# Kernel tuning notes

Measured on AMD Instinct MI355X. Metric: run time of the kernel, lower is better.

The kernel has to match this reference:

```python
import jax, jax.numpy as jnp
import numpy as np

T, B, N = 12, 2, 1024
M = B * N            # nodes per timestep (batch-flattened)
D_IN, D_H, D_T, D_O = 64, 128, 16, 32


def _linear_params(k, fin, fout):
    kw, kb = jax.random.split(k)
    s = 1.0 / np.sqrt(fin)
    w = jax.random.uniform(kw, (fin, fout), jnp.float32, -s, s)
    b = jax.random.uniform(kb, (fout,), jnp.float32, -s, s)
    return w, b


def setup_inputs() -> dict:
    key = jax.random.key(0)
    ks = jax.random.split(key, 12)
    x = jax.random.normal(ks[0], (T, M, D_IN), jnp.float32)
    A = (jax.random.uniform(ks[1], (T, M, M)) < 0.01).astype(jnp.float32)
    A = A * (1.0 - jnp.eye(M, dtype=jnp.float32))  # no self-loops in raw adjacency
    ego_mask = jax.random.randint(ks[2], (B, T, N), 0, 2).astype(bool)
    gcn1_w, gcn1_b = _linear_params(ks[3], D_IN, D_H)
    gcn2_w, gcn2_b = _linear_params(ks[4], D_H, D_H)
    time_w, time_b = _linear_params(ks[5], 1, D_T)
    q_w, q_b = _linear_params(ks[6], D_H + D_T, D_H)
    k_w, k_b = _linear_params(ks[7], D_H + D_T, D_H)
    v_w, v_b = _linear_params(ks[8], D_H + D_T, D_H)
    o_w, o_b = _linear_params(ks[9], D_H, D_H)
    fc_w, fc_b = _linear_params(ks[10], D_H, D_O)
    return dict(x=x, A=A, ego_mask=ego_mask,
                gcn1_w=gcn1_w, gcn1_b=gcn1_b, gcn2_w=gcn2_w, gcn2_b=gcn2_b,
                time_w=time_w, time_b=time_b,
                q_w=q_w, q_b=q_b, k_w=k_w, k_b=k_b, v_w=v_w, v_b=v_b,
                o_w=o_w, o_b=o_b, fc_w=fc_w, fc_b=fc_b)


def _forward(x, A, ego_mask, gcn1_w, gcn1_b, gcn2_w, gcn2_b, time_w, time_b,
             q_w, q_b, k_w, k_b, v_w, v_b, o_w, o_b, fc_w, fc_b):
    # [B,T,N] -> [T, B*N], as in mask.permute(1,0,2).reshape(T,-1)
    mask = ego_mask.transpose(1, 0, 2).reshape(T, M)
    tvals = jnp.arange(T, dtype=jnp.float32)

    def step(_, inp):
        xt, At, mt, tv = inp  # [M,D_IN], [M,M], [M] bool, scalar
        m = mt.astype(xt.dtype)
        # restrict adjacency to masked subgraph; GCNConv adds self-loops
        A_hat = At * (m[:, None] * m[None, :]) + jnp.diag(m)
        deg = A_hat.sum(axis=0)  # in-degree per target (PyG gcn_norm on col)
        nrm = jnp.where(deg > 0, 1.0 / jnp.sqrt(jnp.maximum(deg, 1e-12)), 0.0)

        def gcn(h, w, b):
            # out[i] = nrm[i] * sum_j A_hat[j,i] * nrm[j] * (hW)[j] + b
            return (A_hat.T @ ((h @ w) * nrm[:, None])) * nrm[:, None] + b

        h = jax.nn.relu(gcn(xt, gcn1_w, gcn1_b))
        h = jax.nn.relu(gcn(h, gcn2_w, gcn2_b))
        # t_vec = sin(Linear(1,D_T)(t)) -- identical for all nodes
        t_vec = jnp.sin(tv * time_w[0] + time_b)  # [D_T]
        xtc = jnp.concatenate([h, jnp.broadcast_to(t_vec, (M, D_T))], axis=-1)
        Q = xtc @ q_w + q_b
        K = xtc @ k_w + k_b
        V = xtc @ v_w + v_b
        scores = (Q @ K.T) * (1.0 / np.sqrt(D_H))  # [M,M]
        scores = jnp.where(mt[None, :], scores, -1e9)  # keys restricted to mask
        agg = jax.nn.softmax(scores, axis=-1) @ V
        out = ((agg @ o_w + o_b) @ fc_w + fc_b) * m[:, None]  # scatter-back == mask
        return None, out

    _, outs = jax.lax.scan(step, None, (x, A, mask, tvals))  # [T,M,D_O]
    return outs.reshape(T, B, N, D_O).transpose(1, 2, 0, 3)  # [B,N,T,D_O]


def reference(x, A, ego_mask, gcn1_w, gcn1_b, gcn2_w, gcn2_b, time_w, time_b,
              q_w, q_b, k_w, k_b, v_w, v_b, o_w, o_b, fc_w, fc_b):
    return _forward(x, A, ego_mask, gcn1_w, gcn1_b, gcn2_w, gcn2_b, time_w,
                    time_b, q_w, q_b, k_w, k_b, v_w, v_b, o_w, o_b, fc_w, fc_b)
```

## Files before the change

kernel.cpp:

```cpp
#include <hip/hip_runtime.h>
#include <stdint.h>

#define TT   12
#define BB   2
#define NN   1024
#define MM   2048
#define TM   24576
#define DIN  64
#define DH   128
#define DOUT 32
#define CAP  64
#define OUTSZ 786432
#define PWB  292

typedef __attribute__((ext_vector_type(8))) short short8;
typedef __attribute__((ext_vector_type(4))) short short4v;
typedef __attribute__((ext_vector_type(4))) float f32x4;

#define MFMA(a,b,c) __builtin_amdgcn_mfma_f32_16x16x32_bf16((a),(b),(c),0,0,0)

__device__ __forceinline__ float bf2f(unsigned short u){
  union { uint32_t i; float f; } x; x.i = ((uint32_t)u) << 16; return x.f;
}
__device__ __forceinline__ unsigned short f2bf(float f){
  union { float f; uint32_t i; } x; x.f = f;
  uint32_t u = x.i + 0x7FFFu + ((x.i >> 16) & 1u);
  return (unsigned short)(u >> 16);
}
__device__ __forceinline__ float LD(const void* p, size_t i, int mode){
  return mode ? ((const float*)p)[i] : bf2f(((const unsigned short*)p)[i]);
}
__device__ __forceinline__ short8 ldx8(const void* x, size_t off, int md){
  if(md){
    const float4* xf = (const float4*)((const float*)x + off);
    float4 a = xf[0], b = xf[1];
    short8 o;
    o[0]=(short)f2bf(a.x); o[1]=(short)f2bf(a.y); o[2]=(short)f2bf(a.z); o[3]=(short)f2bf(a.w);
    o[4]=(short)f2bf(b.x); o[5]=(short)f2bf(b.y); o[6]=(short)f2bf(b.z); o[7]=(short)f2bf(b.w);
    return o;
  }
  return *(const short8*)((const unsigned short*)x + off);
}

__global__ void k_fill(float* __restrict__ out, int n, float val){
  int i = blockIdx.x*blockDim.x + threadIdx.x;
  if(i < n) out[i] = val;
}

__global__ __launch_bounds__(256) void k_maskdet(
    const void* __restrict__ egom, const unsigned short* __restrict__ xs,
    int* __restrict__ dtf,
    int* __restrict__ cnt, int* __restrict__ nact,
    int* __restrict__ aidx, int* __restrict__ inv,
    float* __restrict__ out)
{
  const int bid = blockIdx.x, tid = threadIdx.x;
  out[(size_t)bid*256 + tid] = 0.f;
  if(bid > TT) return;
  if(bid == TT){
    __shared__ int cnt_s;
    if(tid == 0) cnt_s = 0;
    __syncthreads();
    int c = 0;
    for(int i = tid; i < 6144; i += 256){
      unsigned short hh = xs[i*2];
      unsigned e = (hh >> 7) & 0xFF;
      if(hh==0 || (e >= 0x60 && e <= 0x9F)) c++;
    }
    if(c) atomicAdd(&cnt_s, c);
    __syncthreads();
    if(tid == 0) *dtf = (cnt_s > 4000) ? 0 : 1;
    return;
  }
  const int t = bid, lane = tid & 63, wv = tid >> 6;

  __shared__ int pres_s, ge2_s, wcnt_s[4];
  if(tid == 0){ pres_s = 0; ge2_s = 0; }
  __syncthreads();
  {
    int pres = 0, ge2 = 0;
    const unsigned char* egp = (const unsigned char*)egom;
    for(int i = tid; i < 24576; i += 256){
      unsigned v = egp[i];
      if(v){ pres |= 1 << (i & 7); if(v >= 2u) ge2 = 1; }
    }
    if(pres) atomicOr(&pres_s, pres);
    if(ge2)  atomicOr(&ge2_s, 1);
  }
  __syncthreads();
  int mode;
  {
    int pr = pres_s, g2 = ge2_s;
    if(!g2){
      if((pr & ~0x01) == 0)      mode = 4;
      else if((pr & ~0x11) == 0) mode = 0;
      else                       mode = 1;
    } else {
      if((pr & ~0xC0) == 0)      mode = 5;
      else if((pr & ~0xCC) == 0) mode = 3;
      else                       mode = 2;
    }
  }

  int base = 0;
  for(int r = 0; r < 8; r++){
    int node = r*256 + tid;
    int b = node / NN, n = node % NN;
    int src = (b*TT + t)*NN + n;
    int v;
    if(mode==0)      v = ((const int*)egom)[src] != 0;
    else if(mode==1) v = ((const unsigned char*)egom)[src] != 0;
    else if(mode==2) v = ((const unsigned short*)egom)[src] != 0;
    else if(mode==3) v = ((const float*)egom)[src] != 0.f;
    else if(mode==4) v = ((const long long*)egom)[src] != 0;
    else             v = ((const double*)egom)[src] != 0.0;
    cnt[(size_t)t*MM + node] = 0;
    unsigned long long bal = __ballot(v != 0);
    if(lane == 0) wcnt_s[wv] = __popcll(bal);
    __syncthreads();
    int mybase = base;
    for(int w2 = 0; w2 < wv; w2++) mybase += wcnt_s[w2];
    int ic = -1;
    if(v){
      ic = mybase + __popcll(bal & ((1ULL << lane) - 1ULL));
      aidx[(size_t)t*MM + ic] = node;
    }
    inv[(size_t)t*MM + node] = ic;
    base += wcnt_s[0] + wcnt_s[1] + wcnt_s[2] + wcnt_s[3];
    __syncthreads();
  }
  if(tid == 0) nact[t] = base;
}


__device__ __forceinline__ void dev_prepw2_item(int id, int md,
  const void* w2,
  const void* qw, const void* kw, const void* vw,
  const void* qb0, const void* kb0, const void* vb0,
  const void* ow, const void* ob, const void* fw, const void* fb,
  const void* tw, const void* tb, const void* b1, const void* b2,
  unsigned short* W2t,
  unsigned short* Wqt, unsigned short* Wkt,
  unsigned short* Wvt, unsigned short* Wct,
  float* qbf, float* kbf, float* vbf,
  float* bcf, float* b1f, float* b2f)
{
  if(id < 16384){ int n=id&127,k2=id>>7; W2t[n*128+k2]=f2bf(LD(w2,(size_t)k2*128+n,md)); return; }
  id -= 16384;
  if(id < 16384){ int n=id&127,k2=id>>7; Wqt[n*128+k2]=f2bf(LD(qw,(size_t)k2*128+n,md)); return; }
  id -= 16384;
  if(id < 16384){ int n=id&127,k2=id>>7; Wkt[n*128+k2]=f2bf(LD(kw,(size_t)k2*128+n,md)); return; }
  id -= 16384;
  if(id < 16384){ int n=id&127,k2=id>>7; Wvt[n*128+k2]=f2bf(LD(vw,(size_t)k2*128+n,md)); return; }
  id -= 16384;
  if(id < 4096){
    int oc=id&31, c=id>>5; float s=0.f;
    for(int r=0;r<128;r++) s += LD(ow,(size_t)c*128+r,md)*LD(fw,(size_t)r*32+oc,md);
    Wct[oc*128+c]=f2bf(s); return;
  }
  id -= 4096;
  if(id < 32){
    float s = LD(fb,id,md);
    for(int r=0;r<128;r++) s += LD(ob,r,md)*LD(fw,(size_t)r*32+id,md);
    bcf[id]=s; return;
  }
  id -= 32;
  if(id < 4608){
    int which = id/1536, rem=id%1536, t=rem/128, n=rem%128;
    const void* W  = which==0?qw:(which==1?kw:vw);
    const void* Bs = which==0?qb0:(which==1?kb0:vb0);
    float s = LD(Bs,n,md);
    for(int d=0;d<16;d++){
      float tv = sinf((float)t*LD(tw,d,md) + LD(tb,d,md));
      s += tv * LD(W,(size_t)(128+d)*128+n,md);
    }
    float* dst = which==0?qbf:(which==1?kbf:vbf);
    dst[t*128+n]=s; return;
  }
  id -= 4608;
  if(id < 256){
    if(id<128) b1f[id] = LD(b1,id,md);
    else       b2f[id-128] = LD(b2,id-128,md);
    return;
  }
}

__device__ __forceinline__ void dev_edges_item(int id, int md,
    const void* A, const int* inv, int* cnt, int* edges){
  int lane = id & 63; int row = id >> 6;
  int t = row / MM;
  int jc = inv[row];
  if(jc < 0) return;
  const int* invt = inv + (size_t)t*MM;
  int* cb = cnt + (size_t)t*MM;
  int* eb = edges + (size_t)t*MM*CAP;
  if(md){
    const float4* p4 = (const float4*)((const float*)A + (size_t)row*MM);
    #pragma unroll
    for(int u=0;u<8;u++){
      float4 v = p4[u*64 + lane];
      float wd[4]={v.x,v.y,v.z,v.w};
      #pragma unroll
      for(int q=0;q<4;q++){
        if(wd[q]!=0.f){
          int ibc = invt[(u*64 + lane)*4 + q];
          if(ibc >= 0){ int s=atomicAdd(&cb[ibc],1); if(s<CAP) eb[(size_t)ibc*CAP+s]=jc; }
        }
      }
    }
  } else {
    const uint4* p4 = (const uint4*)((const unsigned short*)A + (size_t)row*MM);
    #pragma unroll
    for(int u=0;u<4;u++){
      uint4 v = p4[u*64 + lane];
      unsigned wd[4]={v.x,v.y,v.z,v.w};
      #pragma unroll
      for(int q=0;q<4;q++){
        int ib = (u*64 + lane)*8 + q*2;
        if(wd[q] & 0xFFFFu){
          int ibc = invt[ib];
          if(ibc >= 0){ int s=atomicAdd(&cb[ibc],1); if(s<CAP) eb[(size_t)ibc*CAP+s]=jc; }
        }
        if(wd[q] >> 16){
          int ibc = invt[ib+1];
          if(ibc >= 0){ int s=atomicAdd(&cb[ibc],1); if(s<CAP) eb[(size_t)ibc*CAP+s]=jc; }
        }
      }
    }
  }
}

__device__ __forceinline__ void dev_gemm_x_direct(int tileIdx, int md, int tid,
    const void* x, const int* nact, const int* aidx,
    const void* w1, float* g)
{
  const int tile = tileIdx*64;
  const int t = tile / MM, il = tile % MM;
  const int na = nact[t];
  if(il >= ((na+63)&~63)) return;
  const int wv=tid>>6, lane=tid&63, l15=lane&15, quad=lane>>4;
  const int r0 = tile + (wv>>1)*32;
  const int c0 = (wv&1)*64;
  short8 bf[2][4];
  #pragma unroll
  for(int kk=0;kk<2;kk++)
    #pragma unroll
    for(int nt=0;nt<4;nt++){
      const int col = c0+nt*16+l15;
      short8 o;
      #pragma unroll
      for(int j=0;j<8;j++)
        o[j] = (short)f2bf(LD(w1, (size_t)(kk*32 + quad*8 + j)*DH + col, md));
      bf[kk][nt] = o;
    }
  const int il0 = (r0 % MM) + l15, il1 = (r0 % MM) + 16 + l15;
  const int n0 = aidx[(size_t)t*MM + (il0 < na ? il0 : 0)];
  const int n1 = aidx[(size_t)t*MM + (il1 < na ? il1 : 0)];
  const size_t xb0 = ((size_t)t*MM + n0)*DIN;
  const size_t xb1 = ((size_t)t*MM + n1)*DIN;
  f32x4 z = {0.f,0.f,0.f,0.f};
  f32x4 acc[2][4];
  #pragma unroll
  for(int i=0;i<2;i++){ acc[i][0]=z; acc[i][1]=z; acc[i][2]=z; acc[i][3]=z; }
  #pragma unroll
  for(int kk=0;kk<2;kk++){
    short8 a0 = ldx8(x, xb0 + kk*32 + quad*8, md);
    short8 a1 = ldx8(x, xb1 + kk*32 + quad*8, md);
    #pragma unroll
    for(int nt=0;nt<4;nt++){
      acc[0][nt]=MFMA(a0,bf[kk][nt],acc[0][nt]);
      acc[1][nt]=MFMA(a1,bf[kk][nt],acc[1][nt]);
    }
  }
  #pragma unroll
  for(int mt=0;mt<2;mt++)
    #pragma unroll
    for(int nt=0;nt<4;nt++){
      int col = c0+nt*16+l15;
      #pragma unroll
      for(int r=0;r<4;r++){
        int row = r0 + mt*16 + quad*4 + r;
        g[(size_t)row*DH + col] = acc[mt][nt][r];
      }
    }
}

__global__ __launch_bounds__(256) void k_pex(
  const void* __restrict__ x, const void* __restrict__ A,
  const void* __restrict__ w1, const void* __restrict__ w2,
  const void* __restrict__ qw, const void* __restrict__ kw, const void* __restrict__ vw,
  const void* __restrict__ qb0, const void* __restrict__ kb0, const void* __restrict__ vb0,
  const void* __restrict__ ow, const void* __restrict__ ob,
  const void* __restrict__ fw, const void* __restrict__ fb,
  const void* __restrict__ tw, const void* __restrict__ tb,
  const void* __restrict__ b1, const void* __restrict__ b2,
  const int* __restrict__ dtf,
  const int* __restrict__ inv, int* __restrict__ cnt, int* __restrict__ edges,
  const int* __restrict__ nact, const int* __restrict__ aidx, float* __restrict__ g,
  unsigned short* __restrict__ W2t,
  unsigned short* __restrict__ Wqt, unsigned short* __restrict__ Wkt,
  unsigned short* __restrict__ Wvt, unsigned short* __restrict__ Wct,
  float* __restrict__ qbf, float* __restrict__ kbf, float* __restrict__ vbf,
  float* __restrict__ bcf, float* __restrict__ b1f, float* __restrict__ b2f)
{
  const int tid = threadIdx.x;
  const int md = *dtf;
  const int b = blockIdx.x;
  if(b < PWB){
    dev_prepw2_item(b*256 + tid, md, w2, qw,kw,vw, qb0,kb0,vb0, ow,ob,fw,fb, tw,tb, b1,b2,
                    W2t, Wqt, Wkt, Wvt, Wct, qbf, kbf, vbf, bcf, b1f, b2f);
  } else if(b < PWB + TM*64/256){
    dev_edges_item((b - PWB)*256 + tid, md, A, inv, cnt, edges);
  } else {
    dev_gemm_x_direct(b - PWB - TM*64/256, md, tid, x, nact, aidx, w1, g);
  }
}

__global__ __launch_bounds__(256) void k_gemm_h(const unsigned short* __restrict__ X,
    const unsigned short* __restrict__ Wt, float* __restrict__ g,
    const int* __restrict__ nact)
{
  const int tile = blockIdx.x*64;
  const int t = tile / MM, il = tile % MM;
  const int na = nact[t];
  if(il >= ((na+63)&~63)) return;
  const int tid=threadIdx.x, wv=tid>>6, lane=tid&63, l15=lane&15, quad=lane>>4;
  const int r0 = tile + (wv>>1)*32;
  const int c0 = (wv&1)*64;
  short8 bf[4][4];
  #pragma unroll
  for(int kk=0;kk<4;kk++)
    #pragma unroll
    for(int nt=0;nt<4;nt++)
      bf[kk][nt] = *(const short8*)(Wt + (size_t)(c0+nt*16+l15)*DH + kk*32 + quad*8);
  f32x4 z = {0.f,0.f,0.f,0.f};
  f32x4 acc[2][4];
  #pragma unroll
  for(int i=0;i<2;i++){ acc[i][0]=z; acc[i][1]=z; acc[i][2]=z; acc[i][3]=z; }
  #pragma unroll
  for(int kk=0;kk<4;kk++){
    short8 a0 = *(const short8*)(X + (size_t)(r0+l15)*DH    + kk*32 + quad*8);
    short8 a1 = *(const short8*)(X + (size_t)(r0+16+l15)*DH + kk*32 + quad*8);
    #pragma unroll
    for(int nt=0;nt<4;nt++){
      acc[0][nt]=MFMA(a0,bf[kk][nt],acc[0][nt]);
      acc[1][nt]=MFMA(a1,bf[kk][nt],acc[1][nt]);
    }
  }
  #pragma unroll
  for(int mt=0;mt<2;mt++)
    #pragma unroll
    for(int nt=0;nt<4;nt++){
      int col = c0+nt*16+l15;
      #pragma unroll
      for(int r=0;r<4;r++){
        int row = r0 + mt*16 + quad*4 + r;
        g[(size_t)row*DH + col] = acc[mt][nt][r];
      }
    }
}

__global__ __launch_bounds__(256) void k_gather(const float* __restrict__ g,
    const int* __restrict__ edges, const int* __restrict__ cnt,
    const int* __restrict__ nact, const float* __restrict__ bias,
    unsigned short* __restrict__ h)
{
  int wv = threadIdx.x>>6, lane = threadIdx.x&63;
  int gi = blockIdx.x*4 + wv;
  int t = gi / MM, ic = gi % MM;
  int na = nact[t];
  if(ic >= ((na+63)&~63)) return;
  unsigned int* hp = (unsigned int*)(h + (size_t)gi*DH) + lane;
  if(ic >= na){ *hp = 0; return; }
  float a0=0.f, a1=0.f;
  int cn = cnt[gi]; if(cn>CAP) cn=CAP;
  const int* eb = edges + (size_t)gi*CAP;
  #pragma unroll 2
  for(int e=0;e<cn;e++){
    int jc = eb[e];
    float nj = rsqrtf((float)cnt[(size_t)t*MM+jc] + 1.f);
    float2 gr2 = *(const float2*)(g + ((size_t)t*MM + jc)*DH + 2*lane);
    a0 += nj*gr2.x; a1 += nj*gr2.y;
  }
  float ni = rsqrtf((float)cn + 1.f);
  float2 gs2 = *(const float2*)(g + (size_t)gi*DH + 2*lane);
  float h0 = ni*(a0 + ni*gs2.x) + bias[2*lane];
  float h1 = ni*(a1 + ni*gs2.y) + bias[2*lane+1];
  h0 = h0>0.f?h0:0.f; h1 = h1>0.f?h1:0.f;
  *hp = (unsigned int)f2bf(h0) | ((unsigned int)f2bf(h1) << 16);
}

__global__ __launch_bounds__(256) void k_gemm_qkv(const unsigned short* __restrict__ X,
    const unsigned short* __restrict__ Wq, const unsigned short* __restrict__ Wk,
    const unsigned short* __restrict__ Wv,
    const float* __restrict__ qb, const float* __restrict__ kb, const float* __restrict__ vb,
    unsigned short* __restrict__ Qo, unsigned short* __restrict__ Ko,
    unsigned short* __restrict__ Vtc, const int* __restrict__ nact)
{
  const int tile = blockIdx.x*64;
  const int t = tile / MM, il = tile % MM;
  const int na = nact[t];
  if(il >= ((na+63)&~63)) return;
  const int which = blockIdx.z;
  const unsigned short* Wt = which==0?Wq:(which==1?Wk:Wv);
  const float* bias = which==0?qb:(which==1?kb:vb);
  const int tid=threadIdx.x, wv=tid>>6, lane=tid&63, l15=lane&15, quad=lane>>4;
  const int r0 = tile + (wv>>1)*32;
  const int c0 = (wv&1)*64;
  short8 bf[4][4];
  #pragma unroll
  for(int kk=0;kk<4;kk++)
    #pragma unroll
    for(int nt=0;nt<4;nt++)
      bf[kk][nt] = *(const short8*)(Wt + (size_t)(c0+nt*16+l15)*DH + kk*32 + quad*8);
  f32x4 z = {0.f,0.f,0.f,0.f};
  f32x4 acc[2][4];
  #pragma unroll
  for(int i=0;i<2;i++){ acc[i][0]=z; acc[i][1]=z; acc[i][2]=z; acc[i][3]=z; }
  #pragma unroll
  for(int kk=0;kk<4;kk++){
    short8 a0 = *(const short8*)(X + (size_t)(r0+l15)*DH    + kk*32 + quad*8);
    short8 a1 = *(const short8*)(X + (size_t)(r0+16+l15)*DH + kk*32 + quad*8);
    #pragma unroll
    for(int nt=0;nt<4;nt++){
      acc[0][nt]=MFMA(a0,bf[kk][nt],acc[0][nt]);
      acc[1][nt]=MFMA(a1,bf[kk][nt],acc[1][nt]);
    }
  }
  if(which < 2){
    unsigned short* o = which==0 ? Qo : Ko;
    #pragma unroll
    for(int mt=0;mt<2;mt++)
      #pragma unroll
      for(int nt=0;nt<4;nt++){
        int col = c0+nt*16+l15;
        float bb = bias[t*DH+col];
        #pragma unroll
        for(int r=0;r<4;r++){
          int row = r0 + mt*16 + quad*4 + r;
          o[(size_t)row*DH + col] = f2bf(acc[mt][nt][r] + bb);
        }
      }
  } else {
    #pragma unroll
    for(int mt=0;mt<2;mt++)
      #pragma unroll
      for(int nt=0;nt<4;nt++){
        int col = c0+nt*16+l15;
        float bb = bias[t*DH+col];
        int node0 = il + (wv>>1)*32 + mt*16 + quad*4;
        short4v pk;
        #pragma unroll
        for(int r=0;r<4;r++) pk[r] = (short)f2bf(acc[mt][nt][r] + bb);
        *(short4v*)(Vtc + ((size_t)t*DH + col)*MM + node0) = pk;
      }
  }
}

__global__ __launch_bounds__(256) void k_attn(
  const unsigned short* __restrict__ Q, const unsigned short* __restrict__ Kc,
  const unsigned short* __restrict__ Vtc, const int* __restrict__ nact,
  const int* __restrict__ aidx, const unsigned short* __restrict__ Wct,
  const float* __restrict__ bc, float* __restrict__ out)
{
  __shared__ unsigned short Kl[64][136];
  __shared__ unsigned short Vl[128][72];
  __shared__ short Pl[4][16][72];
  __shared__ short Al[4][16][136];
  const int tid=threadIdx.x, wv=tid>>6, lane=tid&63, l15=lane&15, quad=lane>>4;
  const int t = blockIdx.y;
  const int na = nact[t];
  const int qblk = blockIdx.x*64;
  if(qblk >= na) return;
  const int qbase = qblk + wv*16;
  const float scale = 0.088388347648318447f;
  const int nkt = (na + 63) >> 6;

  short8 bq[4];
  #pragma unroll
  for(int kk=0;kk<4;kk++)
    bq[kk] = *(const short8*)(Q + ((size_t)t*MM + qbase + l15)*DH + kk*32 + quad*8);

  f32x4 zz = {0.f,0.f,0.f,0.f};
  f32x4 accPV[8];
  #pragma unroll
  for(int i=0;i<8;i++) accPV[i]=zz;
  float l_run = 0.f;

  const int srow = tid >> 2, sseg = tid & 3;
  const int vch  = tid >> 1, vhalf = tid & 1;

  short8 kreg[4], vreg[4];
  {
    const unsigned short* gk = Kc + ((size_t)t*MM + srow)*DH + sseg*32;
    const unsigned short* gv = Vtc + ((size_t)t*DH + vch)*MM + vhalf*32;
    #pragma unroll
    for(int j=0;j<4;j++){ kreg[j] = *(const short8*)(gk + j*8);
                          vreg[j] = *(const short8*)(gv + j*8); }
  }

  for(int kt=0; kt<nkt; kt++){
    const int key0 = kt*64;
    __syncthreads();
    {
      short8* kd = (short8*)&Kl[srow][sseg*32];
      short8* vd = (short8*)&Vl[vch][vhalf*32];
      #pragma unroll
      for(int j=0;j<4;j++){ kd[j] = kreg[j]; vd[j] = vreg[j]; }
    }
    __syncthreads();
    if(kt+1 < nkt){
      const int key1 = key0 + 64;
      const unsigned short* gk = Kc + ((size_t)t*MM + key1 + srow)*DH + sseg*32;
      const unsigned short* gv = Vtc + ((size_t)t*DH + vch)*MM + key1 + vhalf*32;
      #pragma unroll
      for(int j=0;j<4;j++){ kreg[j] = *(const short8*)(gk + j*8);
                            vreg[j] = *(const short8*)(gv + j*8); }
    }
    #pragma unroll
    for(int mt=0;mt<4;mt++){
      f32x4 s = zz;
      #pragma unroll
      for(int kk=0;kk<4;kk++){
        short8 ak = *(const short8*)&Kl[mt*16+l15][kk*32 + quad*8];
        s = MFMA(ak, bq[kk], s);
      }
      short4v pk;
      #pragma unroll
      for(int r=0;r<4;r++){
        float sv = fminf(fmaxf(s[r]*scale, -15.f), 15.f);
        float valid = (key0 + mt*16 + quad*4 + r < na) ? 1.f : 0.f;
        float p = __expf(sv) * valid;
        pk[r] = (short)f2bf(p);
        l_run += bf2f((unsigned short)pk[r]);
      }
      *(short4v*)&Pl[wv][l15][mt*16 + quad*4] = pk;
    }
    #pragma unroll
    for(int kk=0;kk<2;kk++){
      short8 ap = *(const short8*)&Pl[wv][l15][kk*32 + quad*8];
      #pragma unroll
      for(int nt=0;nt<8;nt++){
        short8 bv = *(const short8*)&Vl[nt*16+l15][kk*32 + quad*8];
        accPV[nt] = MFMA(ap, bv, accPV[nt]);
      }
    }
  }
  l_run += __shfl_xor(l_run, 16, 64);
  l_run += __shfl_xor(l_run, 32, 64);

  #pragma unroll
  for(int nt=0;nt<8;nt++)
    #pragma unroll
    for(int r=0;r<4;r++){
      float av = fminf(fmaxf(accPV[nt][r], -1e30f), 1e30f);
      Al[wv][quad*4+r][nt*16+l15] = (short)f2bf(av);
    }

  const int qc = qbase + l15;
  const bool qok = (qc < na);
  const float linv = (l_run > 0.f) ? 1.f/l_run : 0.f;
  const int node = aidx[(size_t)t*MM + (qok ? qc : 0)];
  #pragma unroll
  for(int mt2=0;mt2<2;mt2++){
    f32x4 d = zz;
    #pragma unroll
    for(int kk=0;kk<4;kk++){
      short8 aw = *(const short8*)(Wct + (size_t)(mt2*16+l15)*DH + kk*32 + quad*8);
      short8 bl = *(const short8*)&Al[wv][l15][kk*32 + quad*8];
      d = MFMA(aw, bl, d);
    }
    f32x4 bcv = *(const f32x4*)(bc + mt2*16 + quad*4);
    f32x4 o4;
    #pragma unroll
    for(int r=0;r<4;r++) o4[r] = d[r]*linv + bcv[r];
    if(qok)
      *(f32x4*)(out + (size_t)node*(TT*DOUT) + (size_t)t*DOUT + mt2*16 + quad*4) = o4;
  }
}


extern "C" void kernel_launch(void* const* d_in, const int* in_sizes, int n_in,
                              void* d_out, int out_size, void* d_ws, size_t ws_size,
                              hipStream_t stream)
{
  float* outp = (float*)d_out;
  static const int EXP[19] = {1572864,50331648,24576,8192,128,16384,128,16,16,
                              18432,128,18432,128,18432,128,16384,128,4096,32};
  bool ok = (n_in >= 19) && (out_size == OUTSZ);
  if(ok) for(int i=0;i<19;i++) if(in_sizes[i] != EXP[i]) { ok = false; break; }
  if(!ok){
    k_fill<<<(out_size+255)/256,256,0,stream>>>(outp, out_size, 1000.f);
    return;
  }
  const void* x   = d_in[0];
  const void* A   = d_in[1];
  const void* eg  = d_in[2];
  const void* w1  = d_in[3];
  const void* b1  = d_in[4];
  const void* w2  = d_in[5];
  const void* b2  = d_in[6];
  const void* tw  = d_in[7];
  const void* tb  = d_in[8];
  const void* qw  = d_in[9];
  const void* qb0 = d_in[10];
  const void* kw  = d_in[11];
  const void* kb0 = d_in[12];
  const void* vw  = d_in[13];
  const void* vb0 = d_in[14];
  const void* ow  = d_in[15];
  const void* ob  = d_in[16];
  const void* fw  = d_in[17];
  const void* fb  = d_in[18];

  char* w = (char*)d_ws;
  size_t off = 0;
  auto alloc = [&](size_t sz)->char*{
    char* p = w + off; off = (off + sz + 255) & ~(size_t)255; return p; };
  int*   dtf   = (int*)  alloc(4);
  int*   nactb = (int*)  alloc(TT*4);
  int*   cnt   = (int*)  alloc((size_t)TM*4);
  int*   aidx  = (int*)  alloc((size_t)TM*4);
  int*   inv   = (int*)  alloc((size_t)TM*4);
  int*   edges = (int*)  alloc((size_t)TM*CAP*4);
  float* g     = (float*)alloc((size_t)TM*DH*4);
  unsigned short* h   = (unsigned short*)alloc((size_t)TM*DH*2);
  unsigned short* Vtc = (unsigned short*)alloc((size_t)TT*DH*MM*2);
  unsigned short* W2t = (unsigned short*)alloc(DH*DH*2);
  unsigned short* Wqt = (unsigned short*)alloc(DH*DH*2);
  unsigned short* Wkt = (unsigned short*)alloc(DH*DH*2);
  unsigned short* Wvt = (unsigned short*)alloc(DH*DH*2);
  unsigned short* Wct = (unsigned short*)alloc(DOUT*DH*2);
  float* qbf = (float*)alloc(TT*DH*4);
  float* kbf = (float*)alloc(TT*DH*4);
  float* vbf = (float*)alloc(TT*DH*4);
  float* bcf = (float*)alloc(DOUT*4);
  float* b1f = (float*)alloc(DH*4);
  float* b2f = (float*)alloc(DH*4);
  if(off > ws_size){
    k_fill<<<(out_size+255)/256,256,0,stream>>>(outp, out_size, 500.f);
    return;
  }

  unsigned short* Qb = (unsigned short*)g;
  unsigned short* Kb = (unsigned short*)((char*)g + (size_t)TM*DH*2);

  k_maskdet<<<OUTSZ/256,256,0,stream>>>(eg, (const unsigned short*)x, dtf,
                                        cnt, nactb, aidx, inv, outp);
  k_pex<<<PWB + TM*64/256 + TM/64,256,0,stream>>>(
      x, A, w1, w2, qw, kw, vw, qb0, kb0, vb0, ow, ob, fw, fb, tw, tb, b1, b2,
      dtf, inv, cnt, edges, nactb, aidx, g,
      W2t, Wqt, Wkt, Wvt, Wct, qbf, kbf, vbf, bcf, b1f, b2f);
  k_gather<<<TM/4,256,0,stream>>>(g, edges, cnt, nactb, b1f, h);
  k_gemm_h<<<TM/64,256,0,stream>>>(h, W2t, g, nactb);
  k_gather<<<TM/4,256,0,stream>>>(g, edges, cnt, nactb, b2f, h);
  k_gemm_qkv<<<dim3(TM/64,1,3),256,0,stream>>>(h, Wqt,Wkt,Wvt, qbf,kbf,vbf, Qb,Kb,Vtc, nactb);
  k_attn<<<dim3(MM/64,TT),256,0,stream>>>(Qb, Kb, Vtc, nactb, aidx, Wct, bcf, outp);
}
```

Measured before the change: 473.3 us.

## Fuse GCN gather into following GEMMs via LDS tiles and merge QKV passes

```diff
diff --git a/kernel.cpp b/kernel.cpp
--- a/kernel.cpp
+++ b/kernel.cpp
@@ -51,12 +51,9 @@
     const void* __restrict__ egom, const unsigned short* __restrict__ xs,
     int* __restrict__ dtf,
     int* __restrict__ cnt, int* __restrict__ nact,
-    int* __restrict__ aidx, int* __restrict__ inv,
-    float* __restrict__ out)
+    int* __restrict__ aidx, int* __restrict__ inv)
 {
   const int bid = blockIdx.x, tid = threadIdx.x;
-  out[(size_t)bid*256 + tid] = 0.f;
-  if(bid > TT) return;
   if(bid == TT){
     __shared__ int cnt_s;
     if(tid == 0) cnt_s = 0;
@@ -316,16 +313,56 @@
   }
 }
 
-__global__ __launch_bounds__(256) void k_gemm_h(const unsigned short* __restrict__ X,
-    const unsigned short* __restrict__ Wt, float* __restrict__ g,
-    const int* __restrict__ nact)
-{
+__device__ __forceinline__ void dev_gather_tile(int tile, int t, int il, int na,
+    int tid, const float* __restrict__ gsrc, const int* __restrict__ edges,
+    const int* __restrict__ cnt, const float* __restrict__ bias,
+    unsigned short (*Hl)[136])
+{
+  const int wv = tid>>6, lane = tid&63;
+  for(int r = 0; r < 16; r++){
+    const int lrow = wv*16 + r;
+    const int ic = il + lrow;
+    const int gi = t*MM + ic;
+    float h0 = 0.f, h1 = 0.f;
+    if(ic < na){
+      float a0=0.f, a1=0.f;
+      int cn = cnt[gi]; if(cn>CAP) cn=CAP;
+      const int* eb = edges + (size_t)gi*CAP;
+      #pragma unroll 4
+      for(int e=0;e<cn;e++){
+        int jc = eb[e];
+        float nj = rsqrtf((float)cnt[(size_t)t*MM+jc] + 1.f);
+        float2 gr2 = *(const float2*)(gsrc + ((size_t)t*MM + jc)*DH + 2*lane);
+        a0 += nj*gr2.x; a1 += nj*gr2.y;
+      }
+      float ni = rsqrtf((float)cn + 1.f);
+      float2 gs2 = *(const float2*)(gsrc + (size_t)gi*DH + 2*lane);
+      h0 = ni*(a0 + ni*gs2.x) + bias[2*lane];
+      h1 = ni*(a1 + ni*gs2.y) + bias[2*lane+1];
+      h0 = h0>0.f?h0:0.f; h1 = h1>0.f?h1:0.f;
+    }
+    *(unsigned int*)&Hl[lrow][2*lane] =
+        (unsigned int)f2bf(h0) | ((unsigned int)f2bf(h1) << 16);
+  }
+}
+
+__global__ __launch_bounds__(256) void k_gg1(
+    const float* __restrict__ g, const int* __restrict__ edges,
+    const int* __restrict__ cnt, const int* __restrict__ nact,
+    const float* __restrict__ bias, const unsigned short* __restrict__ Wt,
+    float* __restrict__ g2)
+{
+  __shared__ unsigned short Hl[64][136];
+  const int tid = threadIdx.x, wv = tid>>6, lane = tid&63, l15 = lane&15, quad = lane>>4;
   const int tile = blockIdx.x*64;
   const int t = tile / MM, il = tile % MM;
   const int na = nact[t];
   if(il >= ((na+63)&~63)) return;
-  const int tid=threadIdx.x, wv=tid>>6, lane=tid&63, l15=lane&15, quad=lane>>4;
-  const int r0 = tile + (wv>>1)*32;
+
+  dev_gather_tile(tile, t, il, na, tid, g, edges, cnt, bias, Hl);
+  __syncthreads();
+
+  const int r0l = (wv>>1)*32;
   const int c0 = (wv&1)*64;
   short8 bf[4][4];
   #pragma unroll
@@ -339,8 +376,8 @@
   for(int i=0;i<2;i++){ acc[i][0]=z; acc[i][1]=z; acc[i][2]=z; acc[i][3]=z; }
   #pragma unroll
   for(int kk=0;kk<4;kk++){
-    short8 a0 = *(const short8*)(X + (size_t)(r0+l15)*DH    + kk*32 + quad*8);
-    short8 a1 = *(const short8*)(X + (size_t)(r0+16+l15)*DH + kk*32 + quad*8);
+    short8 a0 = *(const short8*)&Hl[r0l+l15   ][kk*32 + quad*8];
+    short8 a1 = *(const short8*)&Hl[r0l+16+l15][kk*32 + quad*8];
     #pragma unroll
     for(int nt=0;nt<4;nt++){
       acc[0][nt]=MFMA(a0,bf[kk][nt],acc[0][nt]);
@@ -354,113 +391,93 @@
       int col = c0+nt*16+l15;
       #pragma unroll
       for(int r=0;r<4;r++){
-        int row = r0 + mt*16 + quad*4 + r;
-        g[(size_t)row*DH + col] = acc[mt][nt][r];
-      }
-    }
-}
-
-__global__ __launch_bounds__(256) void k_gather(const float* __restrict__ g,
-    const int* __restrict__ edges, const int* __restrict__ cnt,
-    const int* __restrict__ nact, const float* __restrict__ bias,
-    unsigned short* __restrict__ h)
-{
-  int wv = threadIdx.x>>6, lane = threadIdx.x&63;
-  int gi = blockIdx.x*4 + wv;
-  int t = gi / MM, ic = gi % MM;
-  int na = nact[t];
-  if(ic >= ((na+63)&~63)) return;
-  unsigned int* hp = (unsigned int*)(h + (size_t)gi*DH) + lane;
-  if(ic >= na){ *hp = 0; return; }
-  float a0=0.f, a1=0.f;
-  int cn = cnt[gi]; if(cn>CAP) cn=CAP;
-  const int* eb = edges + (size_t)gi*CAP;
-  #pragma unroll 2
-  for(int e=0;e<cn;e++){
-    int jc = eb[e];
-    float nj = rsqrtf((float)cnt[(size_t)t*MM+jc] + 1.f);
-    float2 gr2 = *(const float2*)(g + ((size_t)t*MM + jc)*DH + 2*lane);
-    a0 += nj*gr2.x; a1 += nj*gr2.y;
-  }
-  float ni = rsqrtf((float)cn + 1.f);
-  float2 gs2 = *(const float2*)(g + (size_t)gi*DH + 2*lane);
-  float h0 = ni*(a0 + ni*gs2.x) + bias[2*lane];
-  float h1 = ni*(a1 + ni*gs2.y) + bias[2*lane+1];
-  h0 = h0>0.f?h0:0.f; h1 = h1>0.f?h1:0.f;
-  *hp = (unsigned int)f2bf(h0) | ((unsigned int)f2bf(h1) << 16);
-}
-
-__global__ __launch_bounds__(256) void k_gemm_qkv(const unsigned short* __restrict__ X,
+        int row = tile + r0l + mt*16 + quad*4 + r;
+        g2[(size_t)row*DH + col] = acc[mt][nt][r];
+      }
+    }
+}
+
+__global__ __launch_bounds__(256) void k_gqkv(
+    const float* __restrict__ g2, const int* __restrict__ edges,
+    const int* __restrict__ cnt, const int* __restrict__ nact,
+    const float* __restrict__ bias2,
     const unsigned short* __restrict__ Wq, const unsigned short* __restrict__ Wk,
     const unsigned short* __restrict__ Wv,
     const float* __restrict__ qb, const float* __restrict__ kb, const float* __restrict__ vb,
     unsigned short* __restrict__ Qo, unsigned short* __restrict__ Ko,
-    unsigned short* __restrict__ Vtc, const int* __restrict__ nact)
-{
+    unsigned short* __restrict__ Vtc)
+{
+  __shared__ unsigned short Hl[64][136];
+  const int tid = threadIdx.x, wv = tid>>6, lane = tid&63, l15 = lane&15, quad = lane>>4;
   const int tile = blockIdx.x*64;
   const int t = tile / MM, il = tile % MM;
   const int na = nact[t];
   if(il >= ((na+63)&~63)) return;
-  const int which = blockIdx.z;
-  const unsigned short* Wt = which==0?Wq:(which==1?Wk:Wv);
-  const float* bias = which==0?qb:(which==1?kb:vb);
-  const int tid=threadIdx.x, wv=tid>>6, lane=tid&63, l15=lane&15, quad=lane>>4;
-  const int r0 = tile + (wv>>1)*32;
+
+  dev_gather_tile(tile, t, il, na, tid, g2, edges, cnt, bias2, Hl);
+  __syncthreads();
+
+  const int r0l = (wv>>1)*32;
   const int c0 = (wv&1)*64;
-  short8 bf[4][4];
-  #pragma unroll
-  for(int kk=0;kk<4;kk++)
-    #pragma unroll
-    for(int nt=0;nt<4;nt++)
-      bf[kk][nt] = *(const short8*)(Wt + (size_t)(c0+nt*16+l15)*DH + kk*32 + quad*8);
   f32x4 z = {0.f,0.f,0.f,0.f};
-  f32x4 acc[2][4];
-  #pragma unroll
-  for(int i=0;i<2;i++){ acc[i][0]=z; acc[i][1]=z; acc[i][2]=z; acc[i][3]=z; }
-  #pragma unroll
-  for(int kk=0;kk<4;kk++){
-    short8 a0 = *(const short8*)(X + (size_t)(r0+l15)*DH    + kk*32 + quad*8);
-    short8 a1 = *(const short8*)(X + (size_t)(r0+16+l15)*DH + kk*32 + quad*8);
-    #pragma unroll
-    for(int nt=0;nt<4;nt++){
-      acc[0][nt]=MFMA(a0,bf[kk][nt],acc[0][nt]);
-      acc[1][nt]=MFMA(a1,bf[kk][nt],acc[1][nt]);
-    }
-  }
-  if(which < 2){
-    unsigned short* o = which==0 ? Qo : Ko;
-    #pragma unroll
-    for(int mt=0;mt<2;mt++)
+  for(int which = 0; which < 3; which++){
+    const unsigned short* Wt = which==0?Wq:(which==1?Wk:Wv);
+    const float* bias = which==0?qb:(which==1?kb:vb);
+    short8 bf[4][4];
+    #pragma unroll
+    for(int kk=0;kk<4;kk++)
+      #pragma unroll
+      for(int nt=0;nt<4;nt++)
+        bf[kk][nt] = *(const short8*)(Wt + (size_t)(c0+nt*16+l15)*DH + kk*32 + quad*8);
+    f32x4 acc[2][4];
+    #pragma unroll
+    for(int i=0;i<2;i++){ acc[i][0]=z; acc[i][1]=z; acc[i][2]=z; acc[i][3]=z; }
+    #pragma unroll
+    for(int kk=0;kk<4;kk++){
+      short8 a0 = *(const short8*)&Hl[r0l+l15   ][kk*32 + quad*8];
+      short8 a1 = *(const short8*)&Hl[r0l+16+l15][kk*32 + quad*8];
       #pragma unroll
       for(int nt=0;nt<4;nt++){
-        int col = c0+nt*16+l15;
-        float bb = bias[t*DH+col];
+        acc[0][nt]=MFMA(a0,bf[kk][nt],acc[0][nt]);
+        acc[1][nt]=MFMA(a1,bf[kk][nt],acc[1][nt]);
+      }
+    }
+    if(which < 2){
+      unsigned short* o = which==0 ? Qo : Ko;
+      #pragma unroll
+      for(int mt=0;mt<2;mt++)
         #pragma unroll
-        for(int r=0;r<4;r++){
-          int row = r0 + mt*16 + quad*4 + r;
-          o[(size_t)row*DH + col] = f2bf(acc[mt][nt][r] + bb);
+        for(int nt=0;nt<4;nt++){
+          int col = c0+nt*16+l15;
+          float bb = bias[t*DH+col];
+          #pragma unroll
+          for(int r=0;r<4;r++){
+            int row = tile + r0l + mt*16 + quad*4 + r;
+            o[(size_t)row*DH + col] = f2bf(acc[mt][nt][r] + bb);
+          }
         }
-      }
-  } else {
-    #pragma unroll
-    for(int mt=0;mt<2;mt++)
-      #pragma unroll
-      for(int nt=0;nt<4;nt++){
-        int col = c0+nt*16+l15;
-        float bb = bias[t*DH+col];
-        int node0 = il + (wv>>1)*32 + mt*16 + quad*4;
-        short4v pk;
+    } else {
+      #pragma unroll
+      for(int mt=0;mt<2;mt++)
         #pragma unroll
-        for(int r=0;r<4;r++) pk[r] = (short)f2bf(acc[mt][nt][r] + bb);
-        *(short4v*)(Vtc + ((size_t)t*DH + col)*MM + node0) = pk;
-      }
+        for(int nt=0;nt<4;nt++){
+          int col = c0+nt*16+l15;
+          float bb = bias[t*DH+col];
+          int node0 = il + r0l + mt*16 + quad*4;
+          short4v pk;
+          #pragma unroll
+          for(int r=0;r<4;r++) pk[r] = (short)f2bf(acc[mt][nt][r] + bb);
+          *(short4v*)(Vtc + ((size_t)t*DH + col)*MM + node0) = pk;
+        }
+    }
   }
 }
 
 __global__ __launch_bounds__(256) void k_attn(
   const unsigned short* __restrict__ Q, const unsigned short* __restrict__ Kc,
   const unsigned short* __restrict__ Vtc, const int* __restrict__ nact,
-  const int* __restrict__ aidx, const unsigned short* __restrict__ Wct,
+  const int* __restrict__ aidx, const int* __restrict__ inv,
+  const unsigned short* __restrict__ Wct,
   const float* __restrict__ bc, float* __restrict__ out)
 {
   __shared__ unsigned short Kl[64][136];
@@ -471,6 +488,16 @@
   const int t = blockIdx.y;
   const int na = nact[t];
   const int qblk = blockIdx.x*64;
+
+  {
+    int nd = blockIdx.x*64 + (tid >> 2);
+    if(inv[(size_t)t*MM + nd] < 0){
+      f32x4 z4 = {0.f,0.f,0.f,0.f};
+      f32x4* op = (f32x4*)(out + (size_t)nd*(TT*DOUT) + (size_t)t*DOUT);
+      op[(tid&3)*2]   = z4;
+      op[(tid&3)*2+1] = z4;
+    }
+  }
   if(qblk >= na) return;
   const int qbase = qblk + wv*16;
   const float scale = 0.088388347648318447f;
@@ -624,7 +651,7 @@
   int*   inv   = (int*)  alloc((size_t)TM*4);
   int*   edges = (int*)  alloc((size_t)TM*CAP*4);
   float* g     = (float*)alloc((size_t)TM*DH*4);
-  unsigned short* h   = (unsigned short*)alloc((size_t)TM*DH*2);
+  float* g2    = (float*)alloc((size_t)TM*DH*4);
   unsigned short* Vtc = (unsigned short*)alloc((size_t)TT*DH*MM*2);
   unsigned short* W2t = (unsigned short*)alloc(DH*DH*2);
   unsigned short* Wqt = (unsigned short*)alloc(DH*DH*2);
@@ -645,15 +672,15 @@
   unsigned short* Qb = (unsigned short*)g;
   unsigned short* Kb = (unsigned short*)((char*)g + (size_t)TM*DH*2);
 
-  k_maskdet<<<OUTSZ/256,256,0,stream>>>(eg, (const unsigned short*)x, dtf,
-                                        cnt, nactb, aidx, inv, outp);
+  k_maskdet<<<TT+1,256,0,stream>>>(eg, (const unsigned short*)x, dtf,
+                                   cnt, nactb, aidx, inv);
   k_pex<<<PWB + TM*64/256 + TM/64,256,0,stream>>>(
       x, A, w1, w2, qw, kw, vw, qb0, kb0, vb0, ow, ob, fw, fb, tw, tb, b1, b2,
       dtf, inv, cnt, edges, nactb, aidx, g,
       W2t, Wqt, Wkt, Wvt, Wct, qbf, kbf, vbf, bcf, b1f, b2f);
-  k_gather<<<TM/4,256,0,stream>>>(g, edges, cnt, nactb, b1f, h);
-  k_gemm_h<<<TM/64,256,0,stream>>>(h, W2t, g, nactb);
-  k_gather<<<TM/4,256,0,stream>>>(g, edges, cnt, nactb, b2f, h);
-  k_gemm_qkv<<<dim3(TM/64,1,3),256,0,stream>>>(h, Wqt,Wkt,Wvt, qbf,kbf,vbf, Qb,Kb,Vtc, nactb);
-  k_attn<<<dim3(MM/64,TT),256,0,stream>>>(Qb, Kb, Vtc, nactb, aidx, Wct, bcf, outp);
-}
+  k_gg1<<<TM/64,256,0,stream>>>(g, edges, cnt, nactb, b1f, W2t, g2);
+  k_gqkv<<<TM/64,256,0,stream>>>(g2, edges, cnt, nactb, b2f,
+                                 Wqt, Wkt, Wvt, qbf, kbf, vbf, Qb, Kb, Vtc);
+  k_attn<<<dim3(MM/64,TT),256,0,stream>>>(Qb, Kb, Vtc, nactb, aidx, inv,
+                                          Wct, bcf, outp);
+}
```

Result: slower. 567.6 us (+19.9%).
